# Kernel tuning notes

Measured on AMD Instinct MI355X. Metric: run time of the kernel, lower is better.

## Reference

```python
import jax, jax.numpy as jnp
import numpy as np

B, L, D, R = 8, 2048, 512, 512  # batch, seq, feature, n_rules


def setup_inputs() -> dict:
    key = jax.random.key(0)
    ks = jax.random.split(key, 6)
    query = jax.random.normal(ks[0], (B, L, D), dtype=jnp.float32)
    # to_q: Linear(D, D)
    Wq = jax.random.normal(ks[1], (D, D), dtype=jnp.float32) / np.sqrt(D)
    bq = jnp.zeros((D,), dtype=jnp.float32)
    # to_c: Linear(L, R)
    Wc = jax.random.normal(ks[2], (R, L), dtype=jnp.float32) / np.sqrt(L)
    bc = jnp.zeros((R,), dtype=jnp.float32)
    # fuzzy rule params, torch.rand init (uniform [0,1)); widths kept away from 0
    centers = jax.random.uniform(ks[3], (R, D), dtype=jnp.float32)
    widths = jax.random.uniform(ks[4], (R, D), dtype=jnp.float32, minval=0.1, maxval=1.0)
    return {"query": query, "Wq": Wq, "bq": bq, "Wc": Wc, "bc": bc,
            "centers": centers, "widths": widths}


def reference(query, Wq, bq, Wc, bc, centers, widths):
    # q = to_q(query)  (projection=True)
    q = query @ Wq.T + bq  # (B, L, D)
    # z[b,l,r] = -0.5 * mean_d (|q - c| / w)^2 ; abs is a no-op under the square,
    # so expand (q - c)^2 / w^2 into three GEMM-friendly terms (exact same math).
    inv_w2 = 1.0 / (widths * widths)                      # (R, D)
    qq = (q * q) @ inv_w2.T                               # (B, L, R)
    qc = q @ (centers * inv_w2).T                         # (B, L, R)
    cc = jnp.sum(centers * centers * inv_w2, axis=-1)     # (R,)
    z = -(0.5 / D) * (qq - 2.0 * qc + cc)                 # (B, L, R)
    Fss = jax.nn.softmax(z, axis=-1)                      # (B, L, R); dropout p=0
    # conq = to_c applied along the L axis of query, yielding (B, R, D)
    conq = jnp.einsum('bld,rl->brd', query, Wc) + bc[None, :, None]
    return Fss @ conq                                     # (B, L, D)
```

## Files before the change

kernel.cpp:

```cpp
#include <hip/hip_runtime.h>
#include <hip/hip_bf16.h>

constexpr int Bb = 8, Ls = 2048, Dd = 512, Rr = 512;
constexpr int M1 = Bb * Ls;

typedef _Float16 h8v __attribute__((ext_vector_type(8)));
typedef _Float16 h4v __attribute__((ext_vector_type(4)));
typedef float f4v __attribute__((ext_vector_type(4)));

__device__ __forceinline__ void async_copy16(const void* g, void* l) {
  __builtin_amdgcn_global_load_lds((const __attribute__((address_space(1))) unsigned int*)g,
                                   (__attribute__((address_space(3))) unsigned int*)l, 16, 0, 0);
}

__global__ __launch_bounds__(256) void prep_all(
    const float* __restrict__ q, _Float16* __restrict__ qs, _Float16* __restrict__ qt,
    const float* __restrict__ Wq, _Float16* __restrict__ wq,
    const float* __restrict__ Wc, _Float16* __restrict__ wc,
    const float* __restrict__ centers, const float* __restrict__ widths,
    _Float16* __restrict__ iwh, _Float16* __restrict__ c2h, float* __restrict__ cc) {
  const int bid = blockIdx.x, tid = threadIdx.x;
  if (bid < 2048) {
    __shared__ float t[64][65];
    const int b = bid >> 8;
    const int l0 = ((bid >> 3) & 31) * 64;
    const int d0 = (bid & 7) * 64;
    const int r = tid >> 4, c4 = (tid & 15) * 4;
#pragma unroll
    for (int i = 0; i < 4; ++i) {
      const int l = r + i * 16;
      const float4 v = *(const float4*)&q[((long)b * Ls + l0 + l) * Dd + d0 + c4];
      t[l][c4] = v.x; t[l][c4 + 1] = v.y; t[l][c4 + 2] = v.z; t[l][c4 + 3] = v.w;
      h4v h = {(_Float16)v.x, (_Float16)v.y, (_Float16)v.z, (_Float16)v.w};
      *(h4v*)&qs[((long)b * Ls + l0 + l) * Dd + d0 + c4] = h;
    }
    __syncthreads();
#pragma unroll
    for (int i = 0; i < 4; ++i) {
      const int d = r + i * 16;
      h4v h = {(_Float16)t[c4][d], (_Float16)t[c4 + 1][d],
               (_Float16)t[c4 + 2][d], (_Float16)t[c4 + 3][d]};
      *(h4v*)&qt[((long)b * Dd + d0 + d) * Ls + l0 + c4] = h;
    }
  } else if (bid < 2304) {
    const int i = (bid - 2048) * 256 + tid;
    float4 v = *(const float4*)&Wq[(long)i * 4];
    h4v o = {(_Float16)v.x, (_Float16)v.y, (_Float16)v.z, (_Float16)v.w};
    *(h4v*)&wq[(long)i * 4] = o;
  } else if (bid < 3328) {
    const int i = (bid - 2304) * 256 + tid;
    float4 v = *(const float4*)&Wc[(long)i * 4];
    h4v o = {(_Float16)v.x, (_Float16)v.y, (_Float16)v.z, (_Float16)v.w};
    *(h4v*)&wc[(long)i * 4] = o;
  } else {
    const int wave = tid >> 6, lane = tid & 63;
    const int r = (bid - 3328) * 4 + wave;
    float s = 0.f;
#pragma unroll
    for (int j = 0; j < 8; ++j) {
      const int d = j * 64 + lane;
      const float c = centers[(long)r * Dd + d];
      const float w = widths[(long)r * Dd + d];
      const float iw = 1.0f / (w * w);
      iwh[(long)r * Dd + d] = (_Float16)iw;
      c2h[(long)r * Dd + d] = (_Float16)(-2.0f * c * iw);
      s += c * c * iw;
    }
#pragma unroll
    for (int o = 32; o > 0; o >>= 1) s += __shfl_xor(s, o, 64);
    if (lane == 0) cc[r] = s;
  }
}

template <int WM, int EPI>
__device__ __forceinline__ void gemm_body(
    const int lin, const int NX, const int NY, _Float16* __restrict__ smem,
    const _Float16* __restrict__ A, const _Float16* __restrict__ Bm,
    const float* __restrict__ bias, float* __restrict__ Cf, _Float16* __restrict__ Ch,
    const int Kext, const int ldA, const int ldB, const int ldC, const int kstep,
    const long sA, const long sB, const long sC) {
  constexpr int TM = WM * 32;
  _Float16* As = smem;
  _Float16* Bs = smem + TM * 64;

  const int xcd = lin & 7;
  const int wi = lin >> 3;
  const int x = wi % NX;
  const int yy = (wi / NX) * 8 + xcd;
  const int y = yy % NY;
  const int zz = yy / NY;
  const int n0 = x * 128;
  const int m0 = y * TM;
  const int kb = zz * kstep;
  const _Float16* Ab = A + (long)zz * sA;
  const _Float16* Bbp = Bm + (long)zz * sB;

  const int tid = threadIdx.x;
  const int wave = tid >> 6, lane = tid & 63;
  const int wm = wave >> 2, wn = wave & 3;
  const int quad = lane >> 4, tr = lane & 15;
  const int lrow = lane >> 2;
  const int lcol = (lane & 3) * 8;

  f4v acc[WM][2];
#pragma unroll
  for (int i = 0; i < WM; ++i)
#pragma unroll
    for (int j = 0; j < 2; ++j) acc[i][j] = (f4v){0.f, 0.f, 0.f, 0.f};

  for (int k0 = 0; k0 < Kext; k0 += 64) {
    __syncthreads();
#pragma unroll
    for (int c = wave; c < TM / 16; c += 8) {
      const long g = (long)(m0 + c * 16 + lrow) * ldA + kb + k0 + lcol;
      async_copy16(Ab + g, &As[c * 512]);
      async_copy16(Ab + g + 32, &As[TM * 32 + c * 512]);
    }
#pragma unroll
    for (int c = wave; c < 8; c += 8) {
      const long g = (long)(n0 + c * 16 + lrow) * ldB + kb + k0 + lcol;
      async_copy16(Bbp + g, &Bs[c * 512]);
      async_copy16(Bbp + g + 32, &Bs[4096 + c * 512]);
    }
    __syncthreads();

#pragma unroll
    for (int h = 0; h < 2; ++h) {
      h8v af[WM], bf[2];
#pragma unroll
      for (int i = 0; i < WM; ++i)
        af[i] = *(const h8v*)&As[h * (TM * 32) + (wm * (WM * 16) + i * 16 + tr) * 32 + quad * 8];
#pragma unroll
      for (int j = 0; j < 2; ++j)
        bf[j] = *(const h8v*)&Bs[h * 4096 + (wn * 32 + j * 16 + tr) * 32 + quad * 8];
#pragma unroll
      for (int i = 0; i < WM; ++i)
#pragma unroll
        for (int j = 0; j < 2; ++j)
          acc[i][j] = __builtin_amdgcn_mfma_f32_16x16x32_f16(af[i], bf[j], acc[i][j], 0, 0, 0);
    }
  }

  float* Cfb = Cf ? Cf + (long)zz * sC : nullptr;
  _Float16* Chb = Ch ? Ch + (long)zz * sC : nullptr;
#pragma unroll
  for (int i = 0; i < WM; ++i)
#pragma unroll
    for (int j = 0; j < 2; ++j) {
      const int rbase = m0 + wm * (WM * 16) + i * 16 + quad * 4;
      const int cg = n0 + wn * 32 + j * 16 + tr;
#pragma unroll
      for (int r = 0; r < 4; ++r) {
        const float v = acc[i][j][r];
        const long row = rbase + r;
        if (EPI == 2) {
          Chb[row * (long)ldC + cg] = (_Float16)(v + bias[cg]);
        } else if (EPI == 3) {
          Cfb[row * (long)ldC + cg] = v;
        }
      }
    }
}

template <int WM, int EPI>
__global__ __launch_bounds__(512, 4) void gemm_h(
    const _Float16* __restrict__ A, const _Float16* __restrict__ Bm,
    const float* __restrict__ bias, float* __restrict__ Cf,
    _Float16* __restrict__ Ch, int Kext, int ldA, int ldB, int ldC, int kstep,
    long sA, long sB, long sC) {
  extern __shared__ _Float16 smem[];
  const int lin = ((int)blockIdx.z * (int)gridDim.y + (int)blockIdx.y) * (int)gridDim.x +
                  (int)blockIdx.x;
  gemm_body<WM, EPI>(lin, (int)gridDim.x, (int)gridDim.y, smem, A, Bm, bias, Cf, Ch,
                     Kext, ldA, ldB, ldC, kstep, sA, sB, sC);
}

__global__ __launch_bounds__(512, 4) void qgemm_conq(
    const _Float16* __restrict__ qs, const _Float16* __restrict__ wq,
    const float* __restrict__ bq, _Float16* __restrict__ q16,
    const _Float16* __restrict__ qt, const _Float16* __restrict__ wc,
    const float* __restrict__ bc, _Float16* __restrict__ cq) {
  extern __shared__ _Float16 smem[];
  const int bid = (int)blockIdx.x;
  if (bid < 256) {
    gemm_body<2, 2>(bid, 4, 64, smem, qt, wc, bc, nullptr, cq,
                    Ls, Ls, Ls, Rr, 0, 0, 0, 0);
  } else {
    gemm_body<4, 2>(bid - 256, 4, 128, smem, qs, wq, bq, nullptr, q16,
                    Dd, Dd, Dd, Dd, 0, 0, 0, 0);
  }
}

__global__ __launch_bounds__(512, 4) void zq_gemm(
    const _Float16* __restrict__ Q, const _Float16* __restrict__ Iw,
    const _Float16* __restrict__ C2, const float* __restrict__ cc,
    _Float16* __restrict__ Zh) {
  __shared__ _Float16 As[2][128 * 32];
  __shared__ _Float16 B1[2][128 * 32];
  __shared__ _Float16 B2[2][128 * 32];
  const int lin = (int)blockIdx.y * 4 + (int)blockIdx.x;
  const int xcd = lin & 7;
  const int wi = lin >> 3;
  const int x = wi % 4;
  const int yy = (wi / 4) * 8 + xcd;
  const int n0 = x * 128;
  const int m0 = yy * 128;

  const int tid = threadIdx.x;
  const int wave = tid >> 6, lane = tid & 63;
  const int wm = wave >> 2, wn = wave & 3;
  const int quad = lane >> 4, tr = lane & 15;
  const int lrow = lane >> 2;
  const int lcol = (lane & 3) * 8;

  f4v acc[4][2];
#pragma unroll
  for (int i = 0; i < 4; ++i)
#pragma unroll
    for (int j = 0; j < 2; ++j) acc[i][j] = (f4v){0.f, 0.f, 0.f, 0.f};

  for (int k0 = 0; k0 < 512; k0 += 64) {
    __syncthreads();
    {
      const long ga = (long)(m0 + wave * 16 + lrow) * 512 + k0 + lcol;
      async_copy16(Q + ga, &As[0][wave * 512]);
      async_copy16(Q + ga + 32, &As[1][wave * 512]);
      const long gb = (long)(n0 + wave * 16 + lrow) * 512 + k0 + lcol;
      async_copy16(Iw + gb, &B1[0][wave * 512]);
      async_copy16(Iw + gb + 32, &B1[1][wave * 512]);
      async_copy16(C2 + gb, &B2[0][wave * 512]);
      async_copy16(C2 + gb + 32, &B2[1][wave * 512]);
    }
    __syncthreads();

#pragma unroll
    for (int h = 0; h < 2; ++h) {
      h8v af[4], af2[4], b1[2], b2[2];
#pragma unroll
      for (int i = 0; i < 4; ++i) {
        af[i] = *(const h8v*)&As[h][(wm * 64 + i * 16 + tr) * 32 + quad * 8];
        af2[i] = af[i] * af[i];
      }
#pragma unroll
      for (int j = 0; j < 2; ++j) {
        b1[j] = *(const h8v*)&B1[h][(wn * 32 + j * 16 + tr) * 32 + quad * 8];
        b2[j] = *(const h8v*)&B2[h][(wn * 32 + j * 16 + tr) * 32 + quad * 8];
      }
#pragma unroll
      for (int i = 0; i < 4; ++i)
#pragma unroll
        for (int j = 0; j < 2; ++j) {
          acc[i][j] = __builtin_amdgcn_mfma_f32_16x16x32_f16(af2[i], b1[j], acc[i][j], 0, 0, 0);
          acc[i][j] = __builtin_amdgcn_mfma_f32_16x16x32_f16(af[i], b2[j], acc[i][j], 0, 0, 0);
        }
    }
  }

  constexpr float zs = -0.0009765625f;
#pragma unroll
  for (int i = 0; i < 4; ++i)
#pragma unroll
    for (int j = 0; j < 2; ++j) {
      const int rbase = m0 + wm * 64 + i * 16 + quad * 4;
      const int cg = n0 + wn * 32 + j * 16 + tr;
      const float ccv = cc[cg];
#pragma unroll
      for (int r = 0; r < 4; ++r)
        Zh[(long)(rbase + r) * 512 + cg] = (_Float16)((acc[i][j][r] + ccv) * zs);
    }
}

__global__ __launch_bounds__(256) void softmax_h(const _Float16* __restrict__ Zh,
                                                 _Float16* __restrict__ F) {
  const int wave = threadIdx.x >> 6;
  const int lane = threadIdx.x & 63;
  const long row = (long)blockIdx.x * 4 + wave;
  h8v zv = *(const h8v*)&Zh[row * Rr + lane * 8];
  float v[8];
#pragma unroll
  for (int i = 0; i < 8; ++i) v[i] = (float)zv[i];
  float m = v[0];
#pragma unroll
  for (int i = 1; i < 8; ++i) m = fmaxf(m, v[i]);
#pragma unroll
  for (int s = 32; s > 0; s >>= 1) m = fmaxf(m, __shfl_xor(m, s, 64));
  float sum = 0.f;
#pragma unroll
  for (int i = 0; i < 8; ++i) {
    v[i] = __expf(v[i] - m);
    sum += v[i];
  }
#pragma unroll
  for (int s = 32; s > 0; s >>= 1) sum += __shfl_xor(sum, s, 64);
  const float inv = 1.0f / sum;
  h8v o;
#pragma unroll
  for (int i = 0; i < 8; ++i) o[i] = (_Float16)(v[i] * inv);
  *(h8v*)&F[row * Rr + lane * 8] = o;
}

extern "C" void kernel_launch(void* const* d_in, const int* in_sizes, int n_in,
                              void* d_out, int out_size, void* d_ws, size_t ws_size,
                              hipStream_t stream) {
  const float* query   = (const float*)d_in[0];
  const float* Wq      = (const float*)d_in[1];
  const float* bq      = (const float*)d_in[2];
  const float* Wc      = (const float*)d_in[3];
  const float* bc      = (const float*)d_in[4];
  const float* centers = (const float*)d_in[5];
  const float* widths  = (const float*)d_in[6];
  float* out = (float*)d_out;

  char* base = (char*)d_ws;
  auto alloc = [&](size_t bytes) {
    char* p = base;
    base += (bytes + 255) & ~(size_t)255;
    return p;
  };
  _Float16* qs  = (_Float16*)alloc((size_t)M1 * Dd * 2);
  _Float16* qt  = (_Float16*)alloc((size_t)M1 * Dd * 2);
  _Float16* q16 = (_Float16*)alloc((size_t)M1 * Dd * 2);
  _Float16* zh  = (_Float16*)alloc((size_t)M1 * Rr * 2);
  _Float16* fs  = (_Float16*)alloc((size_t)M1 * Rr * 2);
  _Float16* wq  = (_Float16*)alloc((size_t)Dd * Dd * 2);
  _Float16* wc  = (_Float16*)alloc((size_t)Rr * Ls * 2);
  _Float16* iwh = (_Float16*)alloc((size_t)Rr * Dd * 2);
  _Float16* c2h = (_Float16*)alloc((size_t)Rr * Dd * 2);
  float*    cc  = (float*)alloc((size_t)Rr * 4);
  _Float16* cq  = (_Float16*)alloc((size_t)Bb * Dd * Rr * 2);

  prep_all<<<3456, 256, 0, stream>>>(query, qs, qt, Wq, wq, Wc, wc,
                                     centers, widths, iwh, c2h, cc);

  qgemm_conq<<<768, 512, 32768, stream>>>(qs, wq, bq, q16, qt, wc, bc, cq);

  zq_gemm<<<dim3(Rr / 128, M1 / 128, 1), 512, 0, stream>>>(q16, iwh, c2h, cc, zh);

  softmax_h<<<M1 / 4, 256, 0, stream>>>(zh, fs);

  gemm_h<4, 3><<<dim3(Dd / 128, Ls / 128, Bb), 512, 32768, stream>>>(
      fs, cq, nullptr, out, nullptr, Rr, Rr, Rr, Dd, 0,
      (long)Ls * Rr, (long)Dd * Rr, (long)Ls * Dd);
}
```

Before: 172.3 us.

## Fuse softmax exp into Z GEMM epilogue and defer normalization to output GEMM

Result: faster. 163.8 us (-4.9%).

```diff
diff --git a/kernel.cpp b/kernel.cpp
--- a/kernel.cpp
+++ b/kernel.cpp
@@ -18,7 +18,8 @@
     const float* __restrict__ Wq, _Float16* __restrict__ wq,
     const float* __restrict__ Wc, _Float16* __restrict__ wc,
     const float* __restrict__ centers, const float* __restrict__ widths,
-    _Float16* __restrict__ iwh, _Float16* __restrict__ c2h, float* __restrict__ cc) {
+    _Float16* __restrict__ iwh, _Float16* __restrict__ c2h, float* __restrict__ cc,
+    float* __restrict__ rowsum) {
   const int bid = blockIdx.x, tid = threadIdx.x;
   if (bid < 2048) {
     __shared__ float t[64][65];
@@ -52,7 +53,7 @@
     float4 v = *(const float4*)&Wc[(long)i * 4];
     h4v o = {(_Float16)v.x, (_Float16)v.y, (_Float16)v.z, (_Float16)v.w};
     *(h4v*)&wc[(long)i * 4] = o;
-  } else {
+  } else if (bid < 3456) {
     const int wave = tid >> 6, lane = tid & 63;
     const int r = (bid - 3328) * 4 + wave;
     float s = 0.f;
@@ -69,6 +70,9 @@
 #pragma unroll
     for (int o = 32; o > 0; o >>= 1) s += __shfl_xor(s, o, 64);
     if (lane == 0) cc[r] = s;
+  } else {
+    const int i = (bid - 3456) * 256 + tid;
+    ((float4*)rowsum)[i] = (float4){0.f, 0.f, 0.f, 0.f};
   }
 }
 
@@ -144,10 +148,15 @@
   float* Cfb = Cf ? Cf + (long)zz * sC : nullptr;
   _Float16* Chb = Ch ? Ch + (long)zz * sC : nullptr;
 #pragma unroll
-  for (int i = 0; i < WM; ++i)
+  for (int i = 0; i < WM; ++i) {
+    const int rbase = m0 + wm * (WM * 16) + i * 16 + quad * 4;
+    float inv[4];
+    if (EPI == 4) {
+#pragma unroll
+      for (int r = 0; r < 4; ++r) inv[r] = 1.0f / bias[(long)zz * Ls + rbase + r];
+    }
 #pragma unroll
     for (int j = 0; j < 2; ++j) {
-      const int rbase = m0 + wm * (WM * 16) + i * 16 + quad * 4;
       const int cg = n0 + wn * 32 + j * 16 + tr;
 #pragma unroll
       for (int r = 0; r < 4; ++r) {
@@ -157,9 +166,12 @@
           Chb[row * (long)ldC + cg] = (_Float16)(v + bias[cg]);
         } else if (EPI == 3) {
           Cfb[row * (long)ldC + cg] = v;
+        } else if (EPI == 4) {
+          Cfb[row * (long)ldC + cg] = v * inv[r];
         }
       }
     }
+  }
 }
 
 template <int WM, int EPI>
@@ -194,10 +206,11 @@
 __global__ __launch_bounds__(512, 4) void zq_gemm(
     const _Float16* __restrict__ Q, const _Float16* __restrict__ Iw,
     const _Float16* __restrict__ C2, const float* __restrict__ cc,
-    _Float16* __restrict__ Zh) {
+    _Float16* __restrict__ Fh, float* __restrict__ rowsum) {
   __shared__ _Float16 As[2][128 * 32];
   __shared__ _Float16 B1[2][128 * 32];
   __shared__ _Float16 B2[2][128 * 32];
+  __shared__ float rowpart[128][4];
   const int lin = (int)blockIdx.y * 4 + (int)blockIdx.x;
   const int xcd = lin & 7;
   const int wi = lin >> 3;
@@ -258,45 +271,36 @@
 
   constexpr float zs = -0.0009765625f;
 #pragma unroll
-  for (int i = 0; i < 4; ++i)
+  for (int i = 0; i < 4; ++i) {
+    float ps[2][4];
 #pragma unroll
     for (int j = 0; j < 2; ++j) {
-      const int rbase = m0 + wm * 64 + i * 16 + quad * 4;
       const int cg = n0 + wn * 32 + j * 16 + tr;
       const float ccv = cc[cg];
 #pragma unroll
+      for (int r = 0; r < 4; ++r) ps[j][r] = __expf((acc[i][j][r] + ccv) * zs);
+    }
+    const int rbase = m0 + wm * 64 + i * 16 + quad * 4;
+#pragma unroll
+    for (int j = 0; j < 2; ++j) {
+      const int cg = n0 + wn * 32 + j * 16 + tr;
+#pragma unroll
       for (int r = 0; r < 4; ++r)
-        Zh[(long)(rbase + r) * 512 + cg] = (_Float16)((acc[i][j][r] + ccv) * zs);
-    }
-}
-
-__global__ __launch_bounds__(256) void softmax_h(const _Float16* __restrict__ Zh,
-                                                 _Float16* __restrict__ F) {
-  const int wave = threadIdx.x >> 6;
-  const int lane = threadIdx.x & 63;
-  const long row = (long)blockIdx.x * 4 + wave;
-  h8v zv = *(const h8v*)&Zh[row * Rr + lane * 8];
-  float v[8];
-#pragma unroll
-  for (int i = 0; i < 8; ++i) v[i] = (float)zv[i];
-  float m = v[0];
-#pragma unroll
-  for (int i = 1; i < 8; ++i) m = fmaxf(m, v[i]);
-#pragma unroll
-  for (int s = 32; s > 0; s >>= 1) m = fmaxf(m, __shfl_xor(m, s, 64));
-  float sum = 0.f;
-#pragma unroll
-  for (int i = 0; i < 8; ++i) {
-    v[i] = __expf(v[i] - m);
-    sum += v[i];
-  }
-#pragma unroll
-  for (int s = 32; s > 0; s >>= 1) sum += __shfl_xor(sum, s, 64);
-  const float inv = 1.0f / sum;
-  h8v o;
-#pragma unroll
-  for (int i = 0; i < 8; ++i) o[i] = (_Float16)(v[i] * inv);
-  *(h8v*)&F[row * Rr + lane * 8] = o;
+        Fh[(long)(rbase + r) * 512 + cg] = (_Float16)ps[j][r];
+    }
+#pragma unroll
+    for (int r = 0; r < 4; ++r) {
+      float s = ps[0][r] + ps[1][r];
+#pragma unroll
+      for (int o = 8; o > 0; o >>= 1) s += __shfl_xor(s, o, 64);
+      if (tr == 0) rowpart[wm * 64 + i * 16 + quad * 4 + r][wn] = s;
+    }
+  }
+  __syncthreads();
+  if (tid < 128) {
+    const float s = rowpart[tid][0] + rowpart[tid][1] + rowpart[tid][2] + rowpart[tid][3];
+    atomicAdd(&rowsum[m0 + tid], s);
+  }
 }
 
 extern "C" void kernel_launch(void* const* d_in, const int* in_sizes, int n_in,
@@ -320,25 +324,23 @@
   _Float16* qs  = (_Float16*)alloc((size_t)M1 * Dd * 2);
   _Float16* qt  = (_Float16*)alloc((size_t)M1 * Dd * 2);
   _Float16* q16 = (_Float16*)alloc((size_t)M1 * Dd * 2);
-  _Float16* zh  = (_Float16*)alloc((size_t)M1 * Rr * 2);
   _Float16* fs  = (_Float16*)alloc((size_t)M1 * Rr * 2);
   _Float16* wq  = (_Float16*)alloc((size_t)Dd * Dd * 2);
   _Float16* wc  = (_Float16*)alloc((size_t)Rr * Ls * 2);
   _Float16* iwh = (_Float16*)alloc((size_t)Rr * Dd * 2);
   _Float16* c2h = (_Float16*)alloc((size_t)Rr * Dd * 2);
   float*    cc  = (float*)alloc((size_t)Rr * 4);
+  float*    rowsum = (float*)alloc((size_t)M1 * 4);
   _Float16* cq  = (_Float16*)alloc((size_t)Bb * Dd * Rr * 2);
 
-  prep_all<<<3456, 256, 0, stream>>>(query, qs, qt, Wq, wq, Wc, wc,
-                                     centers, widths, iwh, c2h, cc);
+  prep_all<<<3472, 256, 0, stream>>>(query, qs, qt, Wq, wq, Wc, wc,
+                                     centers, widths, iwh, c2h, cc, rowsum);
 
   qgemm_conq<<<768, 512, 32768, stream>>>(qs, wq, bq, q16, qt, wc, bc, cq);
 
-  zq_gemm<<<dim3(Rr / 128, M1 / 128, 1), 512, 0, stream>>>(q16, iwh, c2h, cc, zh);
-
-  softmax_h<<<M1 / 4, 256, 0, stream>>>(zh, fs);
-
-  gemm_h<4, 3><<<dim3(Dd / 128, Ls / 128, Bb), 512, 32768, stream>>>(
-      fs, cq, nullptr, out, nullptr, Rr, Rr, Rr, Dd, 0,
+  zq_gemm<<<dim3(Rr / 128, M1 / 128, 1), 512, 0, stream>>>(q16, iwh, c2h, cc, fs, rowsum);
+
+  gemm_h<4, 4><<<dim3(Dd / 128, Ls / 128, Bb), 512, 32768, stream>>>(
+      fs, cq, rowsum, out, nullptr, Rr, Rr, Rr, Dd, 0,
       (long)Ls * Rr, (long)Dd * Rr, (long)Ls * Dd);
 }
```

## Fuse distance GEMM, softmax and output GEMM into one flash-style kernel

Applied to the files above, without the earlier changes.

Measured after the change: 221.9 us. +28.8%, slower.

```diff
diff --git a/kernel.cpp b/kernel.cpp
--- a/kernel.cpp
+++ b/kernel.cpp
@@ -76,9 +76,8 @@
 __device__ __forceinline__ void gemm_body(
     const int lin, const int NX, const int NY, _Float16* __restrict__ smem,
     const _Float16* __restrict__ A, const _Float16* __restrict__ Bm,
-    const float* __restrict__ bias, float* __restrict__ Cf, _Float16* __restrict__ Ch,
-    const int Kext, const int ldA, const int ldB, const int ldC, const int kstep,
-    const long sA, const long sB, const long sC) {
+    const float* __restrict__ bias, _Float16* __restrict__ Ch,
+    const int Kext, const int ldA, const int ldB, const int ldC) {
   constexpr int TM = WM * 32;
   _Float16* As = smem;
   _Float16* Bs = smem + TM * 64;
@@ -88,12 +87,8 @@
   const int x = wi % NX;
   const int yy = (wi / NX) * 8 + xcd;
   const int y = yy % NY;
-  const int zz = yy / NY;
   const int n0 = x * 128;
   const int m0 = y * TM;
-  const int kb = zz * kstep;
-  const _Float16* Ab = A + (long)zz * sA;
-  const _Float16* Bbp = Bm + (long)zz * sB;
 
   const int tid = threadIdx.x;
   const int wave = tid >> 6, lane = tid & 63;
@@ -112,15 +107,15 @@
     __syncthreads();
 #pragma unroll
     for (int c = wave; c < TM / 16; c += 8) {
-      const long g = (long)(m0 + c * 16 + lrow) * ldA + kb + k0 + lcol;
-      async_copy16(Ab + g, &As[c * 512]);
-      async_copy16(Ab + g + 32, &As[TM * 32 + c * 512]);
+      const long g = (long)(m0 + c * 16 + lrow) * ldA + k0 + lcol;
+      async_copy16(A + g, &As[c * 512]);
+      async_copy16(A + g + 32, &As[TM * 32 + c * 512]);
     }
 #pragma unroll
     for (int c = wave; c < 8; c += 8) {
-      const long g = (long)(n0 + c * 16 + lrow) * ldB + kb + k0 + lcol;
-      async_copy16(Bbp + g, &Bs[c * 512]);
-      async_copy16(Bbp + g + 32, &Bs[4096 + c * 512]);
+      const long g = (long)(n0 + c * 16 + lrow) * ldB + k0 + lcol;
+      async_copy16(Bm + g, &Bs[c * 512]);
+      async_copy16(Bm + g + 32, &Bs[4096 + c * 512]);
     }
     __syncthreads();
 
@@ -141,38 +136,19 @@
     }
   }
 
-  float* Cfb = Cf ? Cf + (long)zz * sC : nullptr;
-  _Float16* Chb = Ch ? Ch + (long)zz * sC : nullptr;
-#pragma unroll
-  for (int i = 0; i < WM; ++i)
+#pragma unroll
+  for (int i = 0; i < WM; ++i) {
+    const int rbase = m0 + wm * (WM * 16) + i * 16 + quad * 4;
 #pragma unroll
     for (int j = 0; j < 2; ++j) {
-      const int rbase = m0 + wm * (WM * 16) + i * 16 + quad * 4;
       const int cg = n0 + wn * 32 + j * 16 + tr;
 #pragma unroll
       for (int r = 0; r < 4; ++r) {
-        const float v = acc[i][j][r];
         const long row = rbase + r;
-        if (EPI == 2) {
-          Chb[row * (long)ldC + cg] = (_Float16)(v + bias[cg]);
-        } else if (EPI == 3) {
-          Cfb[row * (long)ldC + cg] = v;
-        }
-      }
-    }
-}
-
-template <int WM, int EPI>
-__global__ __launch_bounds__(512, 4) void gemm_h(
-    const _Float16* __restrict__ A, const _Float16* __restrict__ Bm,
-    const float* __restrict__ bias, float* __restrict__ Cf,
-    _Float16* __restrict__ Ch, int Kext, int ldA, int ldB, int ldC, int kstep,
-    long sA, long sB, long sC) {
-  extern __shared__ _Float16 smem[];
-  const int lin = ((int)blockIdx.z * (int)gridDim.y + (int)blockIdx.y) * (int)gridDim.x +
-                  (int)blockIdx.x;
-  gemm_body<WM, EPI>(lin, (int)gridDim.x, (int)gridDim.y, smem, A, Bm, bias, Cf, Ch,
-                     Kext, ldA, ldB, ldC, kstep, sA, sB, sC);
+        Ch[row * (long)ldC + cg] = (_Float16)(acc[i][j][r] + bias[cg]);
+      }
+    }
+  }
 }
 
 __global__ __launch_bounds__(512, 4) void qgemm_conq(
@@ -183,120 +159,123 @@
   extern __shared__ _Float16 smem[];
   const int bid = (int)blockIdx.x;
   if (bid < 256) {
-    gemm_body<2, 2>(bid, 4, 64, smem, qt, wc, bc, nullptr, cq,
-                    Ls, Ls, Ls, Rr, 0, 0, 0, 0);
+    gemm_body<2, 2>(bid, 4, 64, smem, qt, wc, bc, cq, Ls, Ls, Ls, Rr);
   } else {
-    gemm_body<4, 2>(bid - 256, 4, 128, smem, qs, wq, bq, nullptr, q16,
-                    Dd, Dd, Dd, Dd, 0, 0, 0, 0);
-  }
-}
-
-__global__ __launch_bounds__(512, 4) void zq_gemm(
+    gemm_body<4, 2>(bid - 256, 4, 128, smem, qs, wq, bq, q16, Dd, Dd, Dd, Dd);
+  }
+}
+
+__global__ __launch_bounds__(512, 4) void zout_fused(
     const _Float16* __restrict__ Q, const _Float16* __restrict__ Iw,
     const _Float16* __restrict__ C2, const float* __restrict__ cc,
-    _Float16* __restrict__ Zh) {
-  __shared__ _Float16 As[2][128 * 32];
-  __shared__ _Float16 B1[2][128 * 32];
-  __shared__ _Float16 B2[2][128 * 32];
-  const int lin = (int)blockIdx.y * 4 + (int)blockIdx.x;
-  const int xcd = lin & 7;
-  const int wi = lin >> 3;
-  const int x = wi % 4;
-  const int yy = (wi / 4) * 8 + xcd;
-  const int n0 = x * 128;
-  const int m0 = yy * 128;
-
-  const int tid = threadIdx.x;
-  const int wave = tid >> 6, lane = tid & 63;
-  const int wm = wave >> 2, wn = wave & 3;
+    const _Float16* __restrict__ cq, float* __restrict__ out) {
+  __shared__ _Float16 A_lds[32 * 512];
+  __shared__ _Float16 P_lds[32 * 128];
+  __shared__ float rowpart[32][8];
+
+  const int blk = (int)blockIdx.x;
+  const int m0 = blk * 32;
+  const int b = blk >> 6;
+  const int tid = threadIdx.x, wave = tid >> 6, lane = tid & 63;
+  const int wn = wave;
   const int quad = lane >> 4, tr = lane & 15;
-  const int lrow = lane >> 2;
-  const int lcol = (lane & 3) * 8;
-
-  f4v acc[4][2];
-#pragma unroll
-  for (int i = 0; i < 4; ++i)
-#pragma unroll
-    for (int j = 0; j < 2; ++j) acc[i][j] = (f4v){0.f, 0.f, 0.f, 0.f};
-
-  for (int k0 = 0; k0 < 512; k0 += 64) {
-    __syncthreads();
-    {
-      const long ga = (long)(m0 + wave * 16 + lrow) * 512 + k0 + lcol;
-      async_copy16(Q + ga, &As[0][wave * 512]);
-      async_copy16(Q + ga + 32, &As[1][wave * 512]);
-      const long gb = (long)(n0 + wave * 16 + lrow) * 512 + k0 + lcol;
-      async_copy16(Iw + gb, &B1[0][wave * 512]);
-      async_copy16(Iw + gb + 32, &B1[1][wave * 512]);
-      async_copy16(C2 + gb, &B2[0][wave * 512]);
-      async_copy16(C2 + gb + 32, &B2[1][wave * 512]);
-    }
-    __syncthreads();
-
-#pragma unroll
-    for (int h = 0; h < 2; ++h) {
-      h8v af[4], af2[4], b1[2], b2[2];
-#pragma unroll
-      for (int i = 0; i < 4; ++i) {
-        af[i] = *(const h8v*)&As[h][(wm * 64 + i * 16 + tr) * 32 + quad * 8];
-        af2[i] = af[i] * af[i];
-      }
-#pragma unroll
-      for (int j = 0; j < 2; ++j) {
-        b1[j] = *(const h8v*)&B1[h][(wn * 32 + j * 16 + tr) * 32 + quad * 8];
-        b2[j] = *(const h8v*)&B2[h][(wn * 32 + j * 16 + tr) * 32 + quad * 8];
-      }
-#pragma unroll
-      for (int i = 0; i < 4; ++i)
-#pragma unroll
-        for (int j = 0; j < 2; ++j) {
-          acc[i][j] = __builtin_amdgcn_mfma_f32_16x16x32_f16(af2[i], b1[j], acc[i][j], 0, 0, 0);
-          acc[i][j] = __builtin_amdgcn_mfma_f32_16x16x32_f16(af[i], b2[j], acc[i][j], 0, 0, 0);
-        }
-    }
-  }
+
+#pragma unroll
+  for (int U = tid; U < 2048; U += 512) {
+    const int row = U >> 6, u = U & 63;
+    async_copy16(Q + (long)(m0 + row) * 512 + (u ^ (row & 15)) * 8, &A_lds[U * 8]);
+  }
+
+  f4v oacc[2][4];
+#pragma unroll
+  for (int i = 0; i < 2; ++i)
+#pragma unroll
+    for (int j = 0; j < 4; ++j) oacc[i][j] = (f4v){0.f, 0.f, 0.f, 0.f};
+  float srow[2][4] = {{0.f, 0.f, 0.f, 0.f}, {0.f, 0.f, 0.f, 0.f}};
+
+  __syncthreads();
 
   constexpr float zs = -0.0009765625f;
-#pragma unroll
-  for (int i = 0; i < 4; ++i)
-#pragma unroll
-    for (int j = 0; j < 2; ++j) {
-      const int rbase = m0 + wm * 64 + i * 16 + quad * 4;
-      const int cg = n0 + wn * 32 + j * 16 + tr;
-      const float ccv = cc[cg];
-#pragma unroll
-      for (int r = 0; r < 4; ++r)
-        Zh[(long)(rbase + r) * 512 + cg] = (_Float16)((acc[i][j][r] + ccv) * zs);
-    }
-}
-
-__global__ __launch_bounds__(256) void softmax_h(const _Float16* __restrict__ Zh,
-                                                 _Float16* __restrict__ F) {
-  const int wave = threadIdx.x >> 6;
-  const int lane = threadIdx.x & 63;
-  const long row = (long)blockIdx.x * 4 + wave;
-  h8v zv = *(const h8v*)&Zh[row * Rr + lane * 8];
-  float v[8];
-#pragma unroll
-  for (int i = 0; i < 8; ++i) v[i] = (float)zv[i];
-  float m = v[0];
-#pragma unroll
-  for (int i = 1; i < 8; ++i) m = fmaxf(m, v[i]);
-#pragma unroll
-  for (int s = 32; s > 0; s >>= 1) m = fmaxf(m, __shfl_xor(m, s, 64));
-  float sum = 0.f;
-#pragma unroll
-  for (int i = 0; i < 8; ++i) {
-    v[i] = __expf(v[i] - m);
-    sum += v[i];
-  }
-#pragma unroll
-  for (int s = 32; s > 0; s >>= 1) sum += __shfl_xor(sum, s, 64);
-  const float inv = 1.0f / sum;
-  h8v o;
-#pragma unroll
-  for (int i = 0; i < 8; ++i) o[i] = (_Float16)(v[i] * inv);
-  *(h8v*)&F[row * Rr + lane * 8] = o;
+  for (int rt = 0; rt < 4; ++rt) {
+    f4v zacc[2] = {(f4v){0.f, 0.f, 0.f, 0.f}, (f4v){0.f, 0.f, 0.f, 0.f}};
+    const int nb = rt * 128 + wn * 16 + tr;
+    const long boff = (long)nb * 512;
+#pragma unroll 4
+    for (int k0 = 0; k0 < 512; k0 += 32) {
+      const int uu = (k0 >> 3) + quad;
+      h8v af0 = *(const h8v*)&A_lds[(tr) * 512 + (uu ^ tr) * 8];
+      h8v af1 = *(const h8v*)&A_lds[(16 + tr) * 512 + (uu ^ tr) * 8];
+      h8v b1 = *(const h8v*)&Iw[boff + k0 + quad * 8];
+      h8v b2 = *(const h8v*)&C2[boff + k0 + quad * 8];
+      zacc[0] = __builtin_amdgcn_mfma_f32_16x16x32_f16(af0 * af0, b1, zacc[0], 0, 0, 0);
+      zacc[0] = __builtin_amdgcn_mfma_f32_16x16x32_f16(af0, b2, zacc[0], 0, 0, 0);
+      zacc[1] = __builtin_amdgcn_mfma_f32_16x16x32_f16(af1 * af1, b1, zacc[1], 0, 0, 0);
+      zacc[1] = __builtin_amdgcn_mfma_f32_16x16x32_f16(af1, b2, zacc[1], 0, 0, 0);
+    }
+    const float ccv = cc[nb];
+    float ps[2][4];
+#pragma unroll
+    for (int i = 0; i < 2; ++i)
+#pragma unroll
+      for (int r = 0; r < 4; ++r) {
+        ps[i][r] = __expf((zacc[i][r] + ccv) * zs);
+        srow[i][r] += ps[i][r];
+      }
+    __syncthreads();
+    const int colL = wn * 16 + tr;
+    const int ucol = colL >> 3;
+#pragma unroll
+    for (int i = 0; i < 2; ++i)
+#pragma unroll
+      for (int r = 0; r < 4; ++r) {
+        const int rl = i * 16 + quad * 4 + r;
+        P_lds[rl * 128 + ((ucol ^ (rl & 15)) << 3) + (colL & 7)] = (_Float16)ps[i][r];
+      }
+    __syncthreads();
+#pragma unroll
+    for (int kk = 0; kk < 128; kk += 32) {
+      const int uu = (kk >> 3) + quad;
+      h8v pa0 = *(const h8v*)&P_lds[(tr) * 128 + ((uu ^ tr) << 3)];
+      h8v pa1 = *(const h8v*)&P_lds[(16 + tr) * 128 + ((uu ^ tr) << 3)];
+      h8v cb[4];
+#pragma unroll
+      for (int j = 0; j < 4; ++j) {
+        const int n = wn * 64 + j * 16 + tr;
+        cb[j] = *(const h8v*)&cq[((long)b * 512 + n) * 512 + rt * 128 + kk + quad * 8];
+      }
+#pragma unroll
+      for (int j = 0; j < 4; ++j) {
+        oacc[0][j] = __builtin_amdgcn_mfma_f32_16x16x32_f16(pa0, cb[j], oacc[0][j], 0, 0, 0);
+        oacc[1][j] = __builtin_amdgcn_mfma_f32_16x16x32_f16(pa1, cb[j], oacc[1][j], 0, 0, 0);
+      }
+    }
+  }
+
+#pragma unroll
+  for (int i = 0; i < 2; ++i)
+#pragma unroll
+    for (int r = 0; r < 4; ++r) {
+      float s = srow[i][r];
+      s += __shfl_xor(s, 1, 64);
+      s += __shfl_xor(s, 2, 64);
+      s += __shfl_xor(s, 4, 64);
+      s += __shfl_xor(s, 8, 64);
+      if (tr == 0) rowpart[i * 16 + quad * 4 + r][wn] = s;
+    }
+  __syncthreads();
+#pragma unroll
+  for (int i = 0; i < 2; ++i)
+#pragma unroll
+    for (int r = 0; r < 4; ++r) {
+      const int rl = i * 16 + quad * 4 + r;
+      float t = 0.f;
+#pragma unroll
+      for (int w = 0; w < 8; ++w) t += rowpart[rl][w];
+      const float inv = 1.0f / t;
+#pragma unroll
+      for (int j = 0; j < 4; ++j)
+        out[(long)(m0 + rl) * 512 + wn * 64 + j * 16 + tr] = oacc[i][j][r] * inv;
+    }
 }
 
 extern "C" void kernel_launch(void* const* d_in, const int* in_sizes, int n_in,
@@ -320,8 +299,6 @@
   _Float16* qs  = (_Float16*)alloc((size_t)M1 * Dd * 2);
   _Float16* qt  = (_Float16*)alloc((size_t)M1 * Dd * 2);
   _Float16* q16 = (_Float16*)alloc((size_t)M1 * Dd * 2);
-  _Float16* zh  = (_Float16*)alloc((size_t)M1 * Rr * 2);
-  _Float16* fs  = (_Float16*)alloc((size_t)M1 * Rr * 2);
   _Float16* wq  = (_Float16*)alloc((size_t)Dd * Dd * 2);
   _Float16* wc  = (_Float16*)alloc((size_t)Rr * Ls * 2);
   _Float16* iwh = (_Float16*)alloc((size_t)Rr * Dd * 2);
@@ -334,11 +311,5 @@
 
   qgemm_conq<<<768, 512, 32768, stream>>>(qs, wq, bq, q16, qt, wc, bc, cq);
 
-  zq_gemm<<<dim3(Rr / 128, M1 / 128, 1), 512, 0, stream>>>(q16, iwh, c2h, cc, zh);
-
-  softmax_h<<<M1 / 4, 256, 0, stream>>>(zh, fs);
-
-  gemm_h<4, 3><<<dim3(Dd / 128, Ls / 128, Bb), 512, 32768, stream>>>(
-      fs, cq, nullptr, out, nullptr, Rr, Rr, Rr, Dd, 0,
-      (long)Ls * Rr, (long)Dd * Rr, (long)Ls * Dd);
-}
+  zout_fused<<<512, 512, 0, stream>>>(q16, iwh, c2h, cc, cq, out);
+}
```
